# Performance work log

Hardware: AMD Instinct MI355X
Metric: run time of the kernel (lower is better)

The kernel has to match this reference:

```python
import jax, jax.numpy as jnp
import numpy as np

N_NODES = 2048
N_EDGES = 32768
N_IN = 256
MSG_HID = 512
MSG_OUT = 256
N_HID = 512


def _linear_params(key, fan_in, fan_out):
    kw, kb = jax.random.split(key)
    bound = 1.0 / np.sqrt(fan_in)
    W = jax.random.uniform(kw, (fan_out, fan_in), jnp.float32, -bound, bound)
    b = jax.random.uniform(kb, (fan_out,), jnp.float32, -bound, bound)
    return W, b


def setup_inputs() -> dict:
    key = jax.random.key(0)
    ks = jax.random.split(key, 8)
    inputs = jax.random.normal(ks[0], (N_NODES, N_IN), jnp.float32)
    # one-hot incidence matrices built from random receiver/sender node indices
    recv_idx = jax.random.randint(ks[1], (N_EDGES,), 0, N_NODES)
    send_idx = jax.random.randint(ks[2], (N_EDGES,), 0, N_NODES)
    rel_rec = jax.nn.one_hot(recv_idx, N_NODES, dtype=jnp.float32)   # [E, N]
    rel_send = jax.nn.one_hot(send_idx, N_NODES, dtype=jnp.float32)  # [E, N]
    msg_W1, msg_b1 = _linear_params(ks[3], 2 * N_IN, MSG_HID)
    msg_W2, msg_b2 = _linear_params(ks[4], MSG_HID, MSG_OUT)
    out_W1, out_b1 = _linear_params(ks[5], N_IN + MSG_OUT, N_HID)
    out_W2, out_b2 = _linear_params(ks[6], N_HID, N_HID)
    out_W3, out_b3 = _linear_params(ks[7], N_HID, N_IN)
    return {
        'inputs': inputs, 'rel_rec': rel_rec, 'rel_send': rel_send,
        'msg_W1': msg_W1, 'msg_b1': msg_b1, 'msg_W2': msg_W2, 'msg_b2': msg_b2,
        'out_W1': out_W1, 'out_b1': out_b1, 'out_W2': out_W2, 'out_b2': out_b2,
        'out_W3': out_W3, 'out_b3': out_b3,
    }


def reference(inputs, rel_rec, rel_send, msg_W1, msg_b1, msg_W2, msg_b2,
              out_W1, out_b1, out_W2, out_b2, out_W3, out_b3):
    # gather node features to edges via dense one-hot matmuls (as in original)
    receivers = rel_rec @ inputs    # [E, n_in]
    senders = rel_send @ inputs     # [E, n_in]
    pre_msg = jnp.concatenate([senders, receivers], axis=1)  # [E, 2*n_in]
    # edge-message MLP (dropout p=0 -> identity)
    msg = jax.nn.relu(pre_msg @ msg_W1.T + msg_b1)
    msg = jax.nn.relu(msg @ msg_W2.T + msg_b2)               # [E, msg_out]
    # scatter-add messages to receiving nodes: (msg^T @ rel_rec)^T == rel_rec^T @ msg
    agg_msgs = rel_rec.T @ msg                               # [N, msg_out]
    aug_inputs = jnp.concatenate([inputs, agg_msgs], axis=-1)
    # node-update MLP
    pred = jax.nn.relu(aug_inputs @ out_W1.T + out_b1)
    pred = jax.nn.relu(pred @ out_W2.T + out_b2)
    pred = pred @ out_W3.T + out_b3
    return inputs + pred
```

## Files before the change

### kernel.cpp

```cpp
#include <hip/hip_runtime.h>
#include <hip/hip_bf16.h>
#include <stdint.h>

using bf16 = __hip_bfloat16;
typedef short bf16x8 __attribute__((ext_vector_type(8)));
typedef float floatx4 __attribute__((ext_vector_type(4)));

static constexpr int NODES = 2048;
static constexpr int EDGES = 32768;

__device__ inline uint4 cvt8(const float* __restrict__ p) {
    const float4* f = (const float4*)p;
    float4 a = f[0], b = f[1];
    union { uint4 u; bf16 h[8]; } pk;
    pk.h[0] = __float2bfloat16(a.x); pk.h[1] = __float2bfloat16(a.y);
    pk.h[2] = __float2bfloat16(a.z); pk.h[3] = __float2bfloat16(a.w);
    pk.h[4] = __float2bfloat16(b.x); pk.h[5] = __float2bfloat16(b.y);
    pk.h[6] = __float2bfloat16(b.z); pk.h[7] = __float2bfloat16(b.w);
    return pk.u;
}

__global__ __launch_bounds__(256) void zero_agg(float4* __restrict__ p) {
    p[(size_t)blockIdx.x * 256 + threadIdx.x] = float4{0.f, 0.f, 0.f, 0.f};
}

__global__ __launch_bounds__(256) void extract_idx(
    const float* __restrict__ rel_rec, const float* __restrict__ rel_send,
    int* __restrict__ recv_idx, int* __restrict__ send_idx)
{
    const int b = blockIdx.x;
    const int half = b >> 13;
    const int rb = b & 8191;
    const float* mat = half ? rel_send : rel_rec;
    int* out = half ? send_idx : recv_idx;
    const int w = threadIdx.x >> 6;
    const int lane = threadIdx.x & 63;
    const int row = rb * 4 + w;
    if (lane == 0) out[row] = 0;
    const uint4* base = (const uint4*)(mat + (size_t)row * NODES);
    for (int p = 0; p < 8; ++p) {
        uint4 v = base[p * 64 + lane];
        const bool hit = (v.x | v.y | v.z | v.w) != 0u;
        if (hit) {
            int e = v.x ? 0 : (v.y ? 1 : (v.z ? 2 : 3));
            out[row] = p * 256 + lane * 4 + e;
        }
        if (__any(hit)) break;
    }
}

template<int AMODE, int BMODE, int EPI>
__global__ __launch_bounds__(256, 2) void gemm128(
    const bf16* __restrict__ A, const float* __restrict__ Af,
    const float* __restrict__ Bt, const float* __restrict__ bias,
    bf16* __restrict__ Cout, float* __restrict__ OutF,
    const float* __restrict__ inputsF, const float* __restrict__ UV,
    const float* __restrict__ b1v, const int* __restrict__ sidx,
    const int* __restrict__ ridx, const float* __restrict__ aggin,
    float* __restrict__ aggout, int M, int N, int K)
{
    constexpr int BM = 128, BN = 128, BK = 32;
    __shared__ bf16 As[BM * BK];
    __shared__ bf16 Bs[BN * BK];
    __shared__ int sIdx[BM];
    __shared__ int rIdx[BM];

    const int t = threadIdx.x;
    const int m0 = blockIdx.y * BM;
    const int n0 = blockIdx.x * BN;

    if constexpr (AMODE == 3) {
        if (t < BM) {
            sIdx[t] = sidx[m0 + t] & (NODES - 1);
            rIdx[t] = ridx[m0 + t] & (NODES - 1);
        }
        __syncthreads();
    }

    const int sr = t >> 2;
    const int sc = t & 3;

    uint4 ra[2], rb[2];

    auto loadTiles = [&](int kt) {
        const int kk = kt * BK + sc * 8;
#pragma unroll
        for (int p = 0; p < 2; ++p) {
            const int row = p * 64 + sr;
            if constexpr (AMODE == 0) {
                ra[p] = *(const uint4*)(A + (size_t)(m0 + row) * K + kk);
            } else if constexpr (AMODE == 1) {
                ra[p] = cvt8(Af + (size_t)(m0 + row) * K + kk);
            } else if constexpr (AMODE == 2) {
                const float* src = (kk < 256)
                    ? (inputsF + (size_t)(m0 + row) * 256 + kk)
                    : (aggin + (size_t)(m0 + row) * 256 + (kk - 256));
                ra[p] = cvt8(src);
            } else {
                const float4* u = (const float4*)(UV + (size_t)sIdx[row] * 1024 + kk);
                const float4* v = (const float4*)(UV + (size_t)rIdx[row] * 1024 + 512 + kk);
                const float4* c = (const float4*)(b1v + kk);
                float4 u0 = u[0], u1 = u[1], v0 = v[0], v1 = v[1], c0 = c[0], c1 = c[1];
                union { uint4 q; bf16 h[8]; } pk;
                pk.h[0] = __float2bfloat16(fmaxf(u0.x + v0.x + c0.x, 0.f));
                pk.h[1] = __float2bfloat16(fmaxf(u0.y + v0.y + c0.y, 0.f));
                pk.h[2] = __float2bfloat16(fmaxf(u0.z + v0.z + c0.z, 0.f));
                pk.h[3] = __float2bfloat16(fmaxf(u0.w + v0.w + c0.w, 0.f));
                pk.h[4] = __float2bfloat16(fmaxf(u1.x + v1.x + c1.x, 0.f));
                pk.h[5] = __float2bfloat16(fmaxf(u1.y + v1.y + c1.y, 0.f));
                pk.h[6] = __float2bfloat16(fmaxf(u1.z + v1.z + c1.z, 0.f));
                pk.h[7] = __float2bfloat16(fmaxf(u1.w + v1.w + c1.w, 0.f));
                ra[p] = pk.q;
            }
            if constexpr (BMODE == 0) {
                rb[p] = cvt8(Bt + (size_t)(n0 + row) * K + kk);
            } else {
                const int n = n0 + row;
                rb[p] = cvt8(Bt + (size_t)(n & 511) * 512 + (n >> 9) * 256 + kk);
            }
        }
    };

    const int wv = t >> 6;
    const int lane = t & 63;
    const int wm = wv >> 1, wn = wv & 1;
    const int r16 = lane & 15, q = lane >> 4;

    floatx4 acc[4][4] = {};

    loadTiles(0);
    const int KT = K / BK;
    for (int kt = 0; kt < KT; ++kt) {
        __syncthreads();
#pragma unroll
        for (int p = 0; p < 2; ++p) {
            *(uint4*)(&As[(p * 64 + sr) * BK + sc * 8]) = ra[p];
            *(uint4*)(&Bs[(p * 64 + sr) * BK + sc * 8]) = rb[p];
        }
        __syncthreads();
        if (kt + 1 < KT) loadTiles(kt + 1);

        bf16x8 af[4], bfr[4];
#pragma unroll
        for (int i = 0; i < 4; ++i)
            af[i] = *(const bf16x8*)(&As[(wm * 64 + i * 16 + r16) * BK + q * 8]);
#pragma unroll
        for (int j = 0; j < 4; ++j)
            bfr[j] = *(const bf16x8*)(&Bs[(wn * 64 + j * 16 + r16) * BK + q * 8]);
#pragma unroll
        for (int i = 0; i < 4; ++i)
#pragma unroll
            for (int j = 0; j < 4; ++j)
                acc[i][j] = __builtin_amdgcn_mfma_f32_16x16x32_bf16(af[i], bfr[j], acc[i][j], 0, 0, 0);
    }

    float bv[4];
#pragma unroll
    for (int j = 0; j < 4; ++j)
        bv[j] = (EPI == 3) ? 0.f : bias[n0 + wn * 64 + j * 16 + r16];

#pragma unroll
    for (int i = 0; i < 4; ++i) {
        const int rbase = m0 + wm * 64 + i * 16 + q * 4;
#pragma unroll
        for (int j = 0; j < 4; ++j) {
            const int gc = n0 + wn * 64 + j * 16 + r16;
#pragma unroll
            for (int r = 0; r < 4; ++r) {
                float v = acc[i][j][r] + bv[j];
                const int gr = rbase + r;
                if constexpr (EPI == 0) {
                    v = fmaxf(v, 0.0f);
                    Cout[(size_t)gr * N + gc] = __float2bfloat16(v);
                } else if constexpr (EPI == 1) {
                    v = fmaxf(v, 0.0f);
                    atomicAdd(&aggout[(size_t)rIdx[gr - m0] * 256 + gc], v);
                } else if constexpr (EPI == 2) {
                    OutF[(size_t)gr * 256 + gc] = inputsF[(size_t)gr * 256 + gc] + v;
                } else {
                    OutF[(size_t)gr * N + gc] = v;
                }
            }
        }
    }
}

extern "C" void kernel_launch(void* const* d_in, const int* in_sizes, int n_in,
                              void* d_out, int out_size, void* d_ws, size_t ws_size,
                              hipStream_t stream) {
    const float* inputs   = (const float*)d_in[0];
    const float* rel_rec  = (const float*)d_in[1];
    const float* rel_send = (const float*)d_in[2];
    const float* msg_W1   = (const float*)d_in[3];
    const float* msg_b1   = (const float*)d_in[4];
    const float* msg_W2   = (const float*)d_in[5];
    const float* msg_b2   = (const float*)d_in[6];
    const float* out_W1   = (const float*)d_in[7];
    const float* out_b1   = (const float*)d_in[8];
    const float* out_W2   = (const float*)d_in[9];
    const float* out_b2   = (const float*)d_in[10];
    const float* out_W3   = (const float*)d_in[11];
    const float* out_b3   = (const float*)d_in[12];

    char* ws = (char*)d_ws;
    int*   recv_idx = (int*)(ws + 0);
    int*   send_idx = (int*)(ws + 131072);
    float* agg      = (float*)(ws + 262144);
    float* UV       = (float*)(ws + 2359296);
    bf16*  g1       = (bf16*)(ws + 10747904);
    bf16*  g2       = (bf16*)(ws + 12845056);
    if (ws_size < (size_t)15 * 1024 * 1024) return;

    extract_idx<<<16384, 256, 0, stream>>>(rel_rec, rel_send, recv_idx, send_idx);

    zero_agg<<<512, 256, 0, stream>>>((float4*)agg);

    gemm128<1, 1, 3><<<dim3(1024 / 128, NODES / 128), 256, 0, stream>>>(
        nullptr, inputs, msg_W1, nullptr, nullptr, UV,
        nullptr, nullptr, nullptr, nullptr, nullptr, nullptr, nullptr,
        NODES, 1024, 256);

    gemm128<3, 0, 1><<<dim3(256 / 128, EDGES / 128), 256, 0, stream>>>(
        nullptr, nullptr, msg_W2, msg_b2, nullptr, nullptr,
        nullptr, UV, msg_b1, send_idx, recv_idx, nullptr, agg,
        EDGES, 256, 512);

    gemm128<2, 0, 0><<<dim3(512 / 128, NODES / 128), 256, 0, stream>>>(
        nullptr, nullptr, out_W1, out_b1, g1, nullptr,
        inputs, nullptr, nullptr, nullptr, nullptr, agg, nullptr,
        NODES, 512, 512);

    gemm128<0, 0, 0><<<dim3(512 / 128, NODES / 128), 256, 0, stream>>>(
        g1, nullptr, out_W2, out_b2, g2, nullptr,
        nullptr, nullptr, nullptr, nullptr, nullptr, nullptr, nullptr,
        NODES, 512, 512);

    gemm128<0, 0, 2><<<dim3(256 / 128, NODES / 128), 256, 0, stream>>>(
        g2, nullptr, out_W3, out_b3, nullptr, (float*)d_out,
        inputs, nullptr, nullptr, nullptr, nullptr, nullptr, nullptr,
        NODES, 256, 512);
}
```

Baseline: 628.9 us.

## Sort edges by receiver to merge scatter-add atomics in edge GEMM epilogue

Builds a counting-sort permutation of edges by receiver index (histogram, scan, scatter) and has the edge-message GEMM process edges in that order. The epilogue then sums consecutive rows that share a receiver before issuing one atomicAdd. This cuts the atomic traffic into the aggregation buffer. In exchange it adds three small kernels, including a single-block scan, and an indirect index load.

```diff
diff --git a/kernel.cpp b/kernel.cpp
--- a/kernel.cpp
+++ b/kernel.cpp
@@ -20,8 +20,14 @@
     return pk.u;
 }
 
-__global__ __launch_bounds__(256) void zero_agg(float4* __restrict__ p) {
-    p[(size_t)blockIdx.x * 256 + threadIdx.x] = float4{0.f, 0.f, 0.f, 0.f};
+__global__ __launch_bounds__(256) void zero_all(float4* __restrict__ agg,
+                                                int4* __restrict__ cnt) {
+    if (blockIdx.x < 512) {
+        agg[(size_t)blockIdx.x * 256 + threadIdx.x] = float4{0.f, 0.f, 0.f, 0.f};
+    } else {
+        cnt[threadIdx.x * 2]     = int4{0, 0, 0, 0};
+        cnt[threadIdx.x * 2 + 1] = int4{0, 0, 0, 0};
+    }
 }
 
 __global__ __launch_bounds__(256) void extract_idx(
@@ -49,6 +55,40 @@
     }
 }
 
+__global__ __launch_bounds__(256) void hist_recv(const int* __restrict__ recv_idx,
+                                                 int* __restrict__ cnt) {
+    const int e = blockIdx.x * 256 + threadIdx.x;
+    atomicAdd(&cnt[recv_idx[e] & (NODES - 1)], 1);
+}
+
+__global__ __launch_bounds__(256) void scan_offsets(const int* __restrict__ cnt,
+                                                    int* __restrict__ cur) {
+    __shared__ int part[256];
+    const int t = threadIdx.x;
+    int loc[8];
+    int s = 0;
+#pragma unroll
+    for (int i = 0; i < 8; ++i) { loc[i] = s; s += cnt[t * 8 + i]; }
+    part[t] = s;
+    __syncthreads();
+    if (t == 0) {
+        int acc = 0;
+        for (int i = 0; i < 256; ++i) { int v = part[i]; part[i] = acc; acc += v; }
+    }
+    __syncthreads();
+    const int b = part[t];
+#pragma unroll
+    for (int i = 0; i < 8; ++i) cur[t * 8 + i] = b + loc[i];
+}
+
+__global__ __launch_bounds__(256) void scatter_perm(const int* __restrict__ recv_idx,
+                                                    int* __restrict__ cur,
+                                                    int* __restrict__ perm) {
+    const int e = blockIdx.x * 256 + threadIdx.x;
+    const int slot = atomicAdd(&cur[recv_idx[e] & (NODES - 1)], 1);
+    perm[slot & (EDGES - 1)] = e;
+}
+
 template<int AMODE, int BMODE, int EPI>
 __global__ __launch_bounds__(256, 2) void gemm128(
     const bf16* __restrict__ A, const float* __restrict__ Af,
@@ -56,8 +96,9 @@
     bf16* __restrict__ Cout, float* __restrict__ OutF,
     const float* __restrict__ inputsF, const float* __restrict__ UV,
     const float* __restrict__ b1v, const int* __restrict__ sidx,
-    const int* __restrict__ ridx, const float* __restrict__ aggin,
-    float* __restrict__ aggout, int M, int N, int K)
+    const int* __restrict__ ridx, const int* __restrict__ perm,
+    const float* __restrict__ aggin, float* __restrict__ aggout,
+    int M, int N, int K)
 {
     constexpr int BM = 128, BN = 128, BK = 32;
     __shared__ bf16 As[BM * BK];
@@ -71,8 +112,9 @@
 
     if constexpr (AMODE == 3) {
         if (t < BM) {
-            sIdx[t] = sidx[m0 + t] & (NODES - 1);
-            rIdx[t] = ridx[m0 + t] & (NODES - 1);
+            const int pe = perm[m0 + t] & (EDGES - 1);
+            sIdx[t] = sidx[pe] & (NODES - 1);
+            rIdx[t] = ridx[pe] & (NODES - 1);
         }
         __syncthreads();
     }
@@ -161,24 +203,39 @@
 
 #pragma unroll
     for (int i = 0; i < 4; ++i) {
-        const int rbase = m0 + wm * 64 + i * 16 + q * 4;
+        const int lr = wm * 64 + i * 16 + q * 4;
+        const int rbase = m0 + lr;
 #pragma unroll
         for (int j = 0; j < 4; ++j) {
             const int gc = n0 + wn * 64 + j * 16 + r16;
-#pragma unroll
-            for (int r = 0; r < 4; ++r) {
-                float v = acc[i][j][r] + bv[j];
-                const int gr = rbase + r;
-                if constexpr (EPI == 0) {
-                    v = fmaxf(v, 0.0f);
-                    Cout[(size_t)gr * N + gc] = __float2bfloat16(v);
-                } else if constexpr (EPI == 1) {
-                    v = fmaxf(v, 0.0f);
-                    atomicAdd(&aggout[(size_t)rIdx[gr - m0] * 256 + gc], v);
-                } else if constexpr (EPI == 2) {
-                    OutF[(size_t)gr * 256 + gc] = inputsF[(size_t)gr * 256 + gc] + v;
-                } else {
-                    OutF[(size_t)gr * N + gc] = v;
+            if constexpr (EPI == 1) {
+                int curR = rIdx[lr];
+                float run = 0.f;
+#pragma unroll
+                for (int r = 0; r < 4; ++r) {
+                    const float v = fmaxf(acc[i][j][r] + bv[j], 0.f);
+                    const int rr = rIdx[lr + r];
+                    if (rr != curR) {
+                        atomicAdd(&aggout[(size_t)curR * 256 + gc], run);
+                        curR = rr; run = v;
+                    } else {
+                        run += v;
+                    }
+                }
+                atomicAdd(&aggout[(size_t)curR * 256 + gc], run);
+            } else {
+#pragma unroll
+                for (int r = 0; r < 4; ++r) {
+                    float v = acc[i][j][r] + bv[j];
+                    const int gr = rbase + r;
+                    if constexpr (EPI == 0) {
+                        v = fmaxf(v, 0.0f);
+                        Cout[(size_t)gr * N + gc] = __float2bfloat16(v);
+                    } else if constexpr (EPI == 2) {
+                        OutF[(size_t)gr * 256 + gc] = inputsF[(size_t)gr * 256 + gc] + v;
+                    } else if constexpr (EPI == 3) {
+                        OutF[(size_t)gr * N + gc] = v;
+                    }
                 }
             }
         }
@@ -209,34 +266,41 @@
     float* UV       = (float*)(ws + 2359296);
     bf16*  g1       = (bf16*)(ws + 10747904);
     bf16*  g2       = (bf16*)(ws + 12845056);
-    if (ws_size < (size_t)15 * 1024 * 1024) return;
+    int*   perm     = (int*)(ws + 14942208);
+    int*   cnt      = (int*)(ws + 15073280);
+    int*   cur      = (int*)(ws + 15081472);
+    if (ws_size < (size_t)16 * 1024 * 1024) return;
 
     extract_idx<<<16384, 256, 0, stream>>>(rel_rec, rel_send, recv_idx, send_idx);
 
-    zero_agg<<<512, 256, 0, stream>>>((float4*)agg);
+    zero_all<<<513, 256, 0, stream>>>((float4*)agg, (int4*)cnt);
+
+    hist_recv<<<EDGES / 256, 256, 0, stream>>>(recv_idx, cnt);
+    scan_offsets<<<1, 256, 0, stream>>>(cnt, cur);
+    scatter_perm<<<EDGES / 256, 256, 0, stream>>>(recv_idx, cur, perm);
 
     gemm128<1, 1, 3><<<dim3(1024 / 128, NODES / 128), 256, 0, stream>>>(
         nullptr, inputs, msg_W1, nullptr, nullptr, UV,
-        nullptr, nullptr, nullptr, nullptr, nullptr, nullptr, nullptr,
+        nullptr, nullptr, nullptr, nullptr, nullptr, nullptr, nullptr, nullptr,
         NODES, 1024, 256);
 
     gemm128<3, 0, 1><<<dim3(256 / 128, EDGES / 128), 256, 0, stream>>>(
         nullptr, nullptr, msg_W2, msg_b2, nullptr, nullptr,
-        nullptr, UV, msg_b1, send_idx, recv_idx, nullptr, agg,
+        nullptr, UV, msg_b1, send_idx, recv_idx, perm, nullptr, agg,
         EDGES, 256, 512);
 
     gemm128<2, 0, 0><<<dim3(512 / 128, NODES / 128), 256, 0, stream>>>(
         nullptr, nullptr, out_W1, out_b1, g1, nullptr,
-        inputs, nullptr, nullptr, nullptr, nullptr, agg, nullptr,
+        inputs, nullptr, nullptr, nullptr, nullptr, nullptr, agg, nullptr,
         NODES, 512, 512);
 
     gemm128<0, 0, 0><<<dim3(512 / 128, NODES / 128), 256, 0, stream>>>(
         g1, nullptr, out_W2, out_b2, g2, nullptr,
-        nullptr, nullptr, nullptr, nullptr, nullptr, nullptr, nullptr,
+        nullptr, nullptr, nullptr, nullptr, nullptr, nullptr, nullptr, nullptr,
         NODES, 512, 512);
 
     gemm128<0, 0, 2><<<dim3(256 / 128, NODES / 128), 256, 0, stream>>>(
         g2, nullptr, out_W3, out_b3, nullptr, (float*)d_out,
-        inputs, nullptr, nullptr, nullptr, nullptr, nullptr, nullptr,
+        inputs, nullptr, nullptr, nullptr, nullptr, nullptr, nullptr, nullptr,
         NODES, 256, 512);
 }
```

New measurement: 636.2 us. About the same (+1.2%).

## Fuse index extraction, zeroing and first GEMM into one launch; shrink node GEMM tiles

Applied to the files above, without the earlier changes.

Merges the index-extraction, accumulator-zeroing and node-level UV GEMM into a single heterogeneous kernel whose block ranges select the work type, cutting two launches. The GEMM is templated on tile size so the small node-side GEMMs use 64x64 tiles, giving more blocks on the GPU for better occupancy. Smaller tiles lower per-block data reuse, and the fused kernel's GEMM blocks are tied to the shape of the extraction blocks.

```diff
diff --git a/kernel.cpp b/kernel.cpp
--- a/kernel.cpp
+++ b/kernel.cpp
@@ -20,54 +20,29 @@
     return pk.u;
 }
 
-__global__ __launch_bounds__(256) void zero_agg(float4* __restrict__ p) {
-    p[(size_t)blockIdx.x * 256 + threadIdx.x] = float4{0.f, 0.f, 0.f, 0.f};
-}
-
-__global__ __launch_bounds__(256) void extract_idx(
-    const float* __restrict__ rel_rec, const float* __restrict__ rel_send,
-    int* __restrict__ recv_idx, int* __restrict__ send_idx)
-{
-    const int b = blockIdx.x;
-    const int half = b >> 13;
-    const int rb = b & 8191;
-    const float* mat = half ? rel_send : rel_rec;
-    int* out = half ? send_idx : recv_idx;
-    const int w = threadIdx.x >> 6;
-    const int lane = threadIdx.x & 63;
-    const int row = rb * 4 + w;
-    if (lane == 0) out[row] = 0;
-    const uint4* base = (const uint4*)(mat + (size_t)row * NODES);
-    for (int p = 0; p < 8; ++p) {
-        uint4 v = base[p * 64 + lane];
-        const bool hit = (v.x | v.y | v.z | v.w) != 0u;
-        if (hit) {
-            int e = v.x ? 0 : (v.y ? 1 : (v.z ? 2 : 3));
-            out[row] = p * 256 + lane * 4 + e;
-        }
-        if (__any(hit)) break;
-    }
-}
-
-template<int AMODE, int BMODE, int EPI>
-__global__ __launch_bounds__(256, 2) void gemm128(
+template<int BM, int BN, int AMODE, int BMODE, int EPI>
+__device__ __forceinline__ void gemm_body(
     const bf16* __restrict__ A, const float* __restrict__ Af,
     const float* __restrict__ Bt, const float* __restrict__ bias,
     bf16* __restrict__ Cout, float* __restrict__ OutF,
     const float* __restrict__ inputsF, const float* __restrict__ UV,
     const float* __restrict__ b1v, const int* __restrict__ sidx,
     const int* __restrict__ ridx, const float* __restrict__ aggin,
-    float* __restrict__ aggout, int M, int N, int K)
+    float* __restrict__ aggout, int M, int N, int K, int bx, int by)
 {
-    constexpr int BM = 128, BN = 128, BK = 32;
+    constexpr int BK = 32;
+    constexpr int PA = BM / 64;
+    constexpr int PB = BN / 64;
+    constexpr int MI = BM / 32;
+    constexpr int NJ = BN / 32;
     __shared__ bf16 As[BM * BK];
     __shared__ bf16 Bs[BN * BK];
     __shared__ int sIdx[BM];
     __shared__ int rIdx[BM];
 
     const int t = threadIdx.x;
-    const int m0 = blockIdx.y * BM;
-    const int n0 = blockIdx.x * BN;
+    const int m0 = by * BM;
+    const int n0 = bx * BN;
 
     if constexpr (AMODE == 3) {
         if (t < BM) {
@@ -80,12 +55,12 @@
     const int sr = t >> 2;
     const int sc = t & 3;
 
-    uint4 ra[2], rb[2];
+    uint4 ra[PA], rb[PB];
 
     auto loadTiles = [&](int kt) {
         const int kk = kt * BK + sc * 8;
 #pragma unroll
-        for (int p = 0; p < 2; ++p) {
+        for (int p = 0; p < PA; ++p) {
             const int row = p * 64 + sr;
             if constexpr (AMODE == 0) {
                 ra[p] = *(const uint4*)(A + (size_t)(m0 + row) * K + kk);
@@ -112,6 +87,10 @@
                 pk.h[7] = __float2bfloat16(fmaxf(u1.w + v1.w + c1.w, 0.f));
                 ra[p] = pk.q;
             }
+        }
+#pragma unroll
+        for (int p = 0; p < PB; ++p) {
+            const int row = p * 64 + sr;
             if constexpr (BMODE == 0) {
                 rb[p] = cvt8(Bt + (size_t)(n0 + row) * K + kk);
             } else {
@@ -126,45 +105,47 @@
     const int wm = wv >> 1, wn = wv & 1;
     const int r16 = lane & 15, q = lane >> 4;
 
-    floatx4 acc[4][4] = {};
+    floatx4 acc[MI][NJ] = {};
 
     loadTiles(0);
     const int KT = K / BK;
     for (int kt = 0; kt < KT; ++kt) {
         __syncthreads();
 #pragma unroll
-        for (int p = 0; p < 2; ++p) {
+        for (int p = 0; p < PA; ++p)
             *(uint4*)(&As[(p * 64 + sr) * BK + sc * 8]) = ra[p];
+#pragma unroll
+        for (int p = 0; p < PB; ++p)
             *(uint4*)(&Bs[(p * 64 + sr) * BK + sc * 8]) = rb[p];
-        }
         __syncthreads();
         if (kt + 1 < KT) loadTiles(kt + 1);
 
-        bf16x8 af[4], bfr[4];
-#pragma unroll
-        for (int i = 0; i < 4; ++i)
-            af[i] = *(const bf16x8*)(&As[(wm * 64 + i * 16 + r16) * BK + q * 8]);
-#pragma unroll
-        for (int j = 0; j < 4; ++j)
-            bfr[j] = *(const bf16x8*)(&Bs[(wn * 64 + j * 16 + r16) * BK + q * 8]);
-#pragma unroll
-        for (int i = 0; i < 4; ++i)
-#pragma unroll
-            for (int j = 0; j < 4; ++j)
+        bf16x8 af[MI], bfr[NJ];
+#pragma unroll
+        for (int i = 0; i < MI; ++i)
+            af[i] = *(const bf16x8*)(&As[(wm * (BM / 2) + i * 16 + r16) * BK + q * 8]);
+#pragma unroll
+        for (int j = 0; j < NJ; ++j)
+            bfr[j] = *(const bf16x8*)(&Bs[(wn * (BN / 2) + j * 16 + r16) * BK + q * 8]);
+#pragma unroll
+        for (int i = 0; i < MI; ++i)
+#pragma unroll
+            for (int j = 0; j < NJ; ++j)
                 acc[i][j] = __builtin_amdgcn_mfma_f32_16x16x32_bf16(af[i], bfr[j], acc[i][j], 0, 0, 0);
     }
 
-    float bv[4];
-#pragma unroll
-    for (int j = 0; j < 4; ++j)
-        bv[j] = (EPI == 3) ? 0.f : bias[n0 + wn * 64 + j * 16 + r16];
-
-#pragma unroll
-    for (int i = 0; i < 4; ++i) {
-        const int rbase = m0 + wm * 64 + i * 16 + q * 4;
-#pragma unroll
-        for (int j = 0; j < 4; ++j) {
-            const int gc = n0 + wn * 64 + j * 16 + r16;
+    float bv[NJ];
+#pragma unroll
+    for (int j = 0; j < NJ; ++j)
+        bv[j] = (EPI == 3) ? 0.f : bias[n0 + wn * (BN / 2) + j * 16 + r16];
+
+#pragma unroll
+    for (int i = 0; i < MI; ++i) {
+        const int lr = wm * (BM / 2) + i * 16 + q * 4;
+        const int rbase = m0 + lr;
+#pragma unroll
+        for (int j = 0; j < NJ; ++j) {
+            const int gc = n0 + wn * (BN / 2) + j * 16 + r16;
 #pragma unroll
             for (int r = 0; r < 4; ++r) {
                 float v = acc[i][j][r] + bv[j];
@@ -174,7 +155,7 @@
                     Cout[(size_t)gr * N + gc] = __float2bfloat16(v);
                 } else if constexpr (EPI == 1) {
                     v = fmaxf(v, 0.0f);
-                    atomicAdd(&aggout[(size_t)rIdx[gr - m0] * 256 + gc], v);
+                    atomicAdd(&aggout[(size_t)rIdx[lr + r] * 256 + gc], v);
                 } else if constexpr (EPI == 2) {
                     OutF[(size_t)gr * 256 + gc] = inputsF[(size_t)gr * 256 + gc] + v;
                 } else {
@@ -182,6 +163,56 @@
                 }
             }
         }
+    }
+}
+
+template<int BM, int BN, int AMODE, int BMODE, int EPI>
+__global__ __launch_bounds__(256, 2) void gemm_k(
+    const bf16* __restrict__ A, const float* __restrict__ Af,
+    const float* __restrict__ Bt, const float* __restrict__ bias,
+    bf16* __restrict__ Cout, float* __restrict__ OutF,
+    const float* __restrict__ inputsF, const float* __restrict__ UV,
+    const float* __restrict__ b1v, const int* __restrict__ sidx,
+    const int* __restrict__ ridx, const float* __restrict__ aggin,
+    float* __restrict__ aggout, int M, int N, int K)
+{
+    gemm_body<BM, BN, AMODE, BMODE, EPI>(A, Af, Bt, bias, Cout, OutF, inputsF,
+        UV, b1v, sidx, ridx, aggin, aggout, M, N, K, blockIdx.x, blockIdx.y);
+}
+
+__global__ __launch_bounds__(256) void fat_pre(
+    const float* __restrict__ rel_rec, const float* __restrict__ rel_send,
+    int* __restrict__ recv_idx, int* __restrict__ send_idx,
+    float4* __restrict__ agg, const float* __restrict__ inputs,
+    const float* __restrict__ msg_W1, float* __restrict__ UV)
+{
+    const int b = blockIdx.x;
+    if (b < 16384) {
+        const int half = b >> 13;
+        const int rb = b & 8191;
+        const float* mat = half ? rel_send : rel_rec;
+        int* out = half ? send_idx : recv_idx;
+        const int w = threadIdx.x >> 6;
+        const int lane = threadIdx.x & 63;
+        const int row = rb * 4 + w;
+        if (lane == 0) out[row] = 0;
+        const uint4* base = (const uint4*)(mat + (size_t)row * NODES);
+        for (int p = 0; p < 8; ++p) {
+            uint4 v = base[p * 64 + lane];
+            const bool hit = (v.x | v.y | v.z | v.w) != 0u;
+            if (hit) {
+                int e = v.x ? 0 : (v.y ? 1 : (v.z ? 2 : 3));
+                out[row] = p * 256 + lane * 4 + e;
+            }
+            if (__any(hit)) break;
+        }
+    } else if (b < 16896) {
+        agg[(size_t)(b - 16384) * 256 + threadIdx.x] = float4{0.f, 0.f, 0.f, 0.f};
+    } else {
+        const int g = b - 16896;
+        gemm_body<64, 64, 1, 1, 3>(nullptr, inputs, msg_W1, nullptr, nullptr, UV,
+            nullptr, nullptr, nullptr, nullptr, nullptr, nullptr, nullptr,
+            NODES, 1024, 256, g & 15, g >> 4);
     }
 }
 
@@ -209,33 +240,27 @@
     float* UV       = (float*)(ws + 2359296);
     bf16*  g1       = (bf16*)(ws + 10747904);
     bf16*  g2       = (bf16*)(ws + 12845056);
-    if (ws_size < (size_t)15 * 1024 * 1024) return;
-
-    extract_idx<<<16384, 256, 0, stream>>>(rel_rec, rel_send, recv_idx, send_idx);
-
-    zero_agg<<<512, 256, 0, stream>>>((float4*)agg);
-
-    gemm128<1, 1, 3><<<dim3(1024 / 128, NODES / 128), 256, 0, stream>>>(
-        nullptr, inputs, msg_W1, nullptr, nullptr, UV,
-        nullptr, nullptr, nullptr, nullptr, nullptr, nullptr, nullptr,
-        NODES, 1024, 256);
-
-    gemm128<3, 0, 1><<<dim3(256 / 128, EDGES / 128), 256, 0, stream>>>(
+    if (ws_size < (size_t)16 * 1024 * 1024) return;
+
+    fat_pre<<<17408, 256, 0, stream>>>(rel_rec, rel_send, recv_idx, send_idx,
+                                       (float4*)agg, inputs, msg_W1, UV);
+
+    gemm_k<128, 128, 3, 0, 1><<<dim3(2, 256), 256, 0, stream>>>(
         nullptr, nullptr, msg_W2, msg_b2, nullptr, nullptr,
         nullptr, UV, msg_b1, send_idx, recv_idx, nullptr, agg,
         EDGES, 256, 512);
 
-    gemm128<2, 0, 0><<<dim3(512 / 128, NODES / 128), 256, 0, stream>>>(
+    gemm_k<64, 64, 2, 0, 0><<<dim3(8, 32), 256, 0, stream>>>(
         nullptr, nullptr, out_W1, out_b1, g1, nullptr,
         inputs, nullptr, nullptr, nullptr, nullptr, agg, nullptr,
         NODES, 512, 512);
 
-    gemm128<0, 0, 0><<<dim3(512 / 128, NODES / 128), 256, 0, stream>>>(
+    gemm_k<64, 64, 0, 0, 0><<<dim3(8, 32), 256, 0, stream>>>(
         g1, nullptr, out_W2, out_b2, g2, nullptr,
         nullptr, nullptr, nullptr, nullptr, nullptr, nullptr, nullptr,
         NODES, 512, 512);
 
-    gemm128<0, 0, 2><<<dim3(256 / 128, NODES / 128), 256, 0, stream>>>(
+    gemm_k<64, 64, 0, 0, 2><<<dim3(4, 32), 256, 0, stream>>>(
         g2, nullptr, out_W3, out_b3, nullptr, (float*)d_out,
         inputs, nullptr, nullptr, nullptr, nullptr, nullptr, nullptr,
         NODES, 256, 512);
```

After: 602.6 us. -4.2%, faster.
